# Kernel tuning notes

Measured on AMD Instinct MI355X. Metric: run time of the kernel, lower is better.

The kernel has to match this reference:

```python
import jax, jax.numpy as jnp
import numpy as np

B, S = 8, 1024          # 8 prefill sequences of length 1024, packed
HIDDEN = 4096
NH, NKV, HD = 32, 8, 128  # q heads, kv heads, head_dim = hidden // NH
G = NH // NKV             # GQA group size
NUM_BLOCKS, BLOCK_SIZE = 1024, 16
ROPE_THETA = 10000.0


def _apply_rope(q, k, pos):
    # q: [T, NH, HD], k: [T, NKV, HD], pos: [T] int32 (NeoX half-split rotation)
    half = HD // 2
    inv_freq = 1.0 / (ROPE_THETA ** (jnp.arange(0, HD, 2, dtype=jnp.float32) / HD))  # [half]
    ang = pos.astype(jnp.float32)[:, None] * inv_freq  # [T, half]
    cos = jnp.cos(ang)[:, None, :]  # [T, 1, half]
    sin = jnp.sin(ang)[:, None, :]

    def rot(t):
        t1, t2 = t[..., :half], t[..., half:]
        return jnp.concatenate([t1 * cos - t2 * sin, t2 * cos + t1 * sin], axis=-1)

    return rot(q), rot(k)


def setup_inputs() -> dict:
    key = jax.random.key(0)
    k1, k2, k3 = jax.random.split(key, 3)
    T = B * S
    x = jax.random.normal(k1, (T, HIDDEN), dtype=jnp.float32)
    wqkv = jax.random.normal(k2, (HIDDEN, (NH + 2 * NKV) * HD), dtype=jnp.float32) * 0.02
    bqkv = jnp.zeros(((NH + 2 * NKV) * HD,), dtype=jnp.float32)
    wo = jax.random.normal(k3, (NH * HD, HIDDEN), dtype=jnp.float32) * 0.02
    pos_list = jnp.tile(jnp.arange(S, dtype=jnp.int32), B)  # per-token position in its sequence
    # contiguous block allocation: token i of the packed batch -> cache slot i
    slot_mapping = jnp.arange(T, dtype=jnp.int32)  # block = slot // BLOCK_SIZE, offset = slot % BLOCK_SIZE
    k_cache = jnp.zeros((NUM_BLOCKS, BLOCK_SIZE, NKV, HD), dtype=jnp.float32)
    v_cache = jnp.zeros((NUM_BLOCKS, BLOCK_SIZE, NKV, HD), dtype=jnp.float32)
    return {"x": x, "wqkv": wqkv, "bqkv": bqkv, "wo": wo,
            "pos_list": pos_list, "slot_mapping": slot_mapping,
            "k_cache": k_cache, "v_cache": v_cache}


def reference(x, wqkv, bqkv, wo, pos_list, slot_mapping, k_cache, v_cache):
    scale = HD ** -0.5
    T = x.shape[0]
    qkv = x @ wqkv + bqkv  # [T, (NH+2*NKV)*HD]
    q = qkv[:, : NH * HD].reshape(T, NH, HD)
    k = qkv[:, NH * HD: (NH + NKV) * HD].reshape(T, NKV, HD)
    v = qkv[:, (NH + NKV) * HD:].reshape(T, NKV, HD)
    q, k = _apply_rope(q, k, pos_list)

    # varlen causal flash attention over B equal-length sequences (GQA)
    qb = q.reshape(B, S, NKV, G, HD)
    kb = k.reshape(B, S, NKV, HD)
    vb = v.reshape(B, S, NKV, HD)
    scores = jnp.einsum('bqhgd,bkhd->bhgqk', qb, kb) * scale  # [B,NKV,G,S,S]
    causal = jnp.tril(jnp.ones((S, S), dtype=bool))
    scores = jnp.where(causal, scores, jnp.float32(-1e30))
    probs = jax.nn.softmax(scores, axis=-1)
    out = jnp.einsum('bhgqk,bkhd->bqhgd', probs, vb).reshape(T, NH * HD)
    out = out @ wo  # [T, HIDDEN]

    # vectorized _write_to_paged_cache: scatter each token's k/v into its slot
    kc = k_cache.reshape(-1, NKV, HD).at[slot_mapping].set(k).reshape(k_cache.shape)
    vc = v_cache.reshape(-1, NKV, HD).at[slot_mapping].set(v).reshape(v_cache.shape)
    return out, kc, vc
```

## Files before the change

### kernel.cpp

```cpp
#include <hip/hip_runtime.h>

typedef unsigned short u16;
typedef unsigned int   u32;
typedef __attribute__((ext_vector_type(8))) short short8;
typedef __attribute__((ext_vector_type(4))) float f32x4;
typedef __attribute__((ext_vector_type(4))) u16   u16x4;

#define GLOAD16(gp, lp) __builtin_amdgcn_global_load_lds( \
    (const __attribute__((address_space(1))) void*)(gp),   \
    (__attribute__((address_space(3))) void*)(lp), 16, 0, 0)

__device__ __forceinline__ float bf2f(u16 u) {
  union { u32 i; float f; } v; v.i = ((u32)u) << 16; return v.f;
}
__device__ __forceinline__ u16 f2bf(float f) {
  union { float f; u32 i; } v; v.f = f;
  return (u16)((v.i + 0x7fffu + ((v.i >> 16) & 1u)) >> 16);
}

#define TTOK 8192
#define SLEN 1024
#define NBATCH 8
#define NHQ 32
#define NKVH 8
#define HDIM 128
#define QKVW 6144
#define HID 4096

__global__ void ap_copyf4(const f32x4* __restrict__ src, f32x4* __restrict__ dst, int n4) {
  int stride = gridDim.x * 256;
  for (int i = blockIdx.x * 256 + threadIdx.x; i < n4; i += stride) dst[i] = src[i];
}

__global__ void ap_convx(const float* __restrict__ x, u16* __restrict__ xb) {
  size_t e = ((size_t)blockIdx.x * 256 + threadIdx.x) * 8;
  f32x4 a = *(const f32x4*)(x + e);
  f32x4 b = *(const f32x4*)(x + e + 4);
  short8 o;
  o[0]=(short)f2bf(a[0]); o[1]=(short)f2bf(a[1]); o[2]=(short)f2bf(a[2]); o[3]=(short)f2bf(a[3]);
  o[4]=(short)f2bf(b[0]); o[5]=(short)f2bf(b[1]); o[6]=(short)f2bf(b[2]); o[7]=(short)f2bf(b[3]);
  *(short8*)(xb + e) = o;
}

__global__ __launch_bounds__(256) void ap_tconv(const float* __restrict__ src,
                                                u16* __restrict__ dst, int K, int N) {
  __shared__ u16 tile[64][68];
  int nt = N >> 6;
  int tn = blockIdx.x % nt, tk = blockIdx.x / nt;
  int rr = threadIdx.x >> 4, cc = (threadIdx.x & 15) * 4;
#pragma unroll
  for (int i = 0; i < 4; ++i) {
    int row = i * 16 + rr;
    f32x4 v = *(const f32x4*)(src + (size_t)(tk * 64 + row) * N + tn * 64 + cc);
#pragma unroll
    for (int j = 0; j < 4; ++j) tile[row][cc + j] = f2bf(v[j]);
  }
  __syncthreads();
#pragma unroll
  for (int i = 0; i < 4; ++i) {
    int orow = i * 16 + rr;
    u16x4 o;
#pragma unroll
    for (int j = 0; j < 4; ++j) o[j] = tile[cc + j][orow];
    *(u16x4*)(dst + (size_t)(tn * 64 + orow) * K + tk * 64 + cc) = o;
  }
}

__device__ __forceinline__ void ap_stage1k(const u16* __restrict__ g, int ldk,
                                           u16* __restrict__ l, int tid) {
#pragma unroll
  for (int i = 0; i < 2; ++i) {
    int ci = i * 1024 + tid;
    int r = ci >> 3;
    int cb = (ci & 7) * 16;
    int c = (cb ^ ((r & 7) << 4)) >> 1;
    GLOAD16(g + (size_t)r * ldk + c, l + ci * 8);
  }
}

__device__ __forceinline__ short8 ds_frag(const u16* base, int row, int kbyte, int swz) {
  return *(const short8*)((const char*)base + row * 128 + (kbyte ^ swz));
}

template <int OUT_BF16, int HAS_BIAS>
__global__ __launch_bounds__(1024) void ap_gemmw(const u16* __restrict__ A,
                                                 const u16* __restrict__ BT,
                                                 const float* __restrict__ bias,
                                                 void* __restrict__ Cout,
                                                 int M, int N, int K, int nbn) {
  __shared__ u16 sA[2][16384];
  __shared__ u16 sB[2][16384];
  const int tid = threadIdx.x;
  const int wave = tid >> 6, l = tid & 63, l16 = l & 15, lq = l >> 4;
  const int wr = wave >> 2, wc = wave & 3;
  const int swz = (l16 & 7) << 4;

  const int nwg = nbn * (M >> 8);
  const int cpx = nwg >> 3;
  const int wg = (blockIdx.x & 7) * cpx + (blockIdx.x >> 3);
  const int bm = wg / nbn, bn = wg % nbn;

  f32x4 acc[4][4];
  f32x4 zv = {0.f, 0.f, 0.f, 0.f};
#pragma unroll
  for (int mf = 0; mf < 4; ++mf)
#pragma unroll
    for (int nf = 0; nf < 4; ++nf) acc[mf][nf] = zv;

  const u16* Abase = A + (size_t)(bm * 256) * K;
  const u16* Bbase = BT + (size_t)(bn * 256) * K;
  const int NT = K >> 6;

  ap_stage1k(Abase, K, sA[0], tid);
  ap_stage1k(Bbase, K, sB[0], tid);

  for (int kt = 0; kt < NT; ++kt) {
    const u16* sAc = sA[kt & 1];
    const u16* sBc = sB[kt & 1];
    const bool pf = (kt + 1 < NT);

    if (pf) {
      ap_stage1k(Abase + (kt + 1) * 64, K, sA[(kt + 1) & 1], tid);
      ap_stage1k(Bbase + (kt + 1) * 64, K, sB[(kt + 1) & 1], tid);
      asm volatile("s_waitcnt vmcnt(4)" ::: "memory");
    } else {
      asm volatile("s_waitcnt vmcnt(0)" ::: "memory");
    }
    __builtin_amdgcn_s_barrier();
    __builtin_amdgcn_sched_barrier(0);

    {
      short8 bf_[4], af_[4];
#pragma unroll
      for (int nf = 0; nf < 4; ++nf)
        bf_[nf] = ds_frag(sBc, wc * 64 + nf * 16 + l16, lq * 16, swz);
#pragma unroll
      for (int mf = 0; mf < 4; ++mf)
        af_[mf] = ds_frag(sAc, wr * 64 + mf * 16 + l16, lq * 16, swz);
      asm volatile("s_waitcnt lgkmcnt(0)" ::: "memory");
      __builtin_amdgcn_sched_barrier(0);
      __builtin_amdgcn_s_setprio(1);
#pragma unroll
      for (int mf = 0; mf < 4; ++mf)
#pragma unroll
        for (int nf = 0; nf < 4; ++nf)
          acc[mf][nf] = __builtin_amdgcn_mfma_f32_16x16x32_bf16(
              af_[mf], bf_[nf], acc[mf][nf], 0, 0, 0);
      __builtin_amdgcn_s_setprio(0);
    }
    {
      short8 bf_[4], af_[4];
#pragma unroll
      for (int nf = 0; nf < 4; ++nf)
        bf_[nf] = ds_frag(sBc, wc * 64 + nf * 16 + l16, 64 + lq * 16, swz);
#pragma unroll
      for (int mf = 0; mf < 4; ++mf)
        af_[mf] = ds_frag(sAc, wr * 64 + mf * 16 + l16, 64 + lq * 16, swz);
      asm volatile("s_waitcnt lgkmcnt(0)" ::: "memory");
      __builtin_amdgcn_sched_barrier(0);
      __builtin_amdgcn_s_barrier();
      __builtin_amdgcn_s_setprio(1);
#pragma unroll
      for (int mf = 0; mf < 4; ++mf)
#pragma unroll
        for (int nf = 0; nf < 4; ++nf)
          acc[mf][nf] = __builtin_amdgcn_mfma_f32_16x16x32_bf16(
              af_[mf], bf_[nf], acc[mf][nf], 0, 0, 0);
      __builtin_amdgcn_s_setprio(0);
    }
  }

#pragma unroll
  for (int mf = 0; mf < 4; ++mf)
#pragma unroll
    for (int nf = 0; nf < 4; ++nf) {
      int col = bn * 256 + wc * 64 + nf * 16 + l16;
      float bv = HAS_BIAS ? bias[col] : 0.f;
#pragma unroll
      for (int r = 0; r < 4; ++r) {
        int row = bm * 256 + wr * 64 + mf * 16 + lq * 4 + r;
        float v = acc[mf][nf][r] + bv;
        if (OUT_BF16)
          ((u16*)Cout)[(size_t)row * N + col] = f2bf(v);
        else
          ((float*)Cout)[(size_t)row * N + col] = v;
      }
    }
}

__global__ __launch_bounds__(256) void ap_rope(u16* __restrict__ qkv,
                                               const int* __restrict__ pos_list,
                                               const int* __restrict__ slot_mapping,
                                               float* __restrict__ kc) {
  int gid = blockIdx.x * 4 + (threadIdx.x >> 6);
  int i = threadIdx.x & 63;
  int t = gid / 40, head = gid % 40;
  float pos = (float)pos_list[t];
  float inv = expf(-(float)i * 0.14391156516151135f);
  float ang = pos * inv;
  float cs = cosf(ang), sn = sinf(ang);
  int cb = (head < 32) ? head * 128 : 4096 + (head - 32) * 128;
  u16* p = qkv + (size_t)t * QKVW + cb;
  float t1 = bf2f(p[i]), t2 = bf2f(p[i + 64]);
  float o1 = t1 * cs - t2 * sn;
  float o2 = t2 * cs + t1 * sn;
  p[i] = f2bf(o1);
  p[i + 64] = f2bf(o2);
  if (head >= 32) {
    int slot = slot_mapping[t];
    float* kp = kc + (size_t)slot * (NKVH * HDIM) + (head - 32) * 128;
    kp[i] = o1;
    kp[i + 64] = o2;
  }
}

__global__ void ap_vscatter(const u16* __restrict__ qkv,
                            const int* __restrict__ slot_mapping,
                            float* __restrict__ vc) {
  int idx = blockIdx.x * 256 + threadIdx.x;
  int e = idx * 4;
  int t = e >> 10, r = e & 1023;
  int slot = slot_mapping[t];
  u16x4 v = *(const u16x4*)(qkv + (size_t)t * QKVW + 5120 + r);
  f32x4 o;
#pragma unroll
  for (int j = 0; j < 4; ++j) o[j] = bf2f(v[j]);
  *(f32x4*)(vc + (size_t)slot * 1024 + r) = o;
}

__global__ __launch_bounds__(256) void ap_vtrans(const u16* __restrict__ qkv,
                                                 u16* __restrict__ Vt) {
  __shared__ u16 tile[64][68];
  int bid = blockIdx.x;
  int hdt = bid & 1, st = (bid >> 1) & 15, head = bid >> 5;
  int b = head >> 3, h = head & 7;
  int rr = threadIdx.x >> 4, cc = (threadIdx.x & 15) * 4;
#pragma unroll
  for (int i = 0; i < 4; ++i) {
    int s = i * 16 + rr;
    u16x4 v = *(const u16x4*)(qkv + (size_t)(b * 1024 + st * 64 + s) * QKVW + 5120 +
                              h * 128 + hdt * 64 + cc);
#pragma unroll
    for (int j = 0; j < 4; ++j) tile[s][cc + j] = v[j];
  }
  __syncthreads();
#pragma unroll
  for (int i = 0; i < 4; ++i) {
    int hd = i * 16 + rr;
    u16x4 o;
#pragma unroll
    for (int j = 0; j < 4; ++j) o[j] = tile[cc + j][hd];
    *(u16x4*)(Vt + (size_t)head * (HDIM * SLEN) + (size_t)(hdt * 64 + hd) * SLEN +
              st * 64 + cc) = o;
  }
}

__global__ __launch_bounds__(512) void ap_attn4(const u16* __restrict__ qkv,
                                                const u16* __restrict__ Vt,
                                                u16* __restrict__ O) {
  __shared__ u16 sK[64 * 136];
  __shared__ u16 sV[128 * 72];
  __shared__ u16 sP[8 * 32 * 72];
  const int tid = threadIdx.x;
  const int wave = tid >> 6, l = tid & 63, l16 = l & 15, lq = l >> 4;
  const int bid = blockIdx.x;
  const int qt = bid & 15;
  const int kvh = (bid >> 4) & 7;
  const int b = bid >> 7;
  const int qh = kvh * 4 + (wave & 3);
  const int q0 = qt * 64 + (wave >> 2) * 32;
  const int head = b * 8 + kvh;
  const float SC2 = 0.12751649736230717f;

  short8 qf[2][4];
#pragma unroll
  for (int m = 0; m < 2; ++m)
#pragma unroll
    for (int kd = 0; kd < 4; ++kd) {
      size_t t = (size_t)(b * 1024 + q0 + m * 16 + l16);
      qf[m][kd] = *(const short8*)(qkv + t * QKVW + qh * 128 + kd * 32 + lq * 8);
    }

  u16* sPw = sP + wave * 2304;
  f32x4 zv = {0.f, 0.f, 0.f, 0.f};
  f32x4 oacc[2][8];
#pragma unroll
  for (int m = 0; m < 2; ++m)
#pragma unroll
    for (int n = 0; n < 8; ++n) oacc[m][n] = zv;
  float mrun[2][4], lrun[2][4];
#pragma unroll
  for (int m = 0; m < 2; ++m)
#pragma unroll
    for (int r = 0; r < 4; ++r) { mrun[m][r] = -1e30f; lrun[m][r] = 0.f; }

  const int ntiles = qt + 1;
  for (int kt = 0; kt < ntiles; ++kt) {
    const int kv0 = kt * 64;
#pragma unroll
    for (int i = 0; i < 2; ++i) {
      int ci = i * 512 + tid;
      int kr = ci >> 4, ko = (ci & 15) * 8;
      short8 v = *(const short8*)(qkv + (size_t)(b * 1024 + kv0 + kr) * QKVW + 4096 +
                                  kvh * 128 + ko);
      *(short8*)&sK[kr * 136 + ko] = v;
    }
#pragma unroll
    for (int i = 0; i < 2; ++i) {
      int ci = i * 512 + tid;
      int hd = ci >> 3, ko = (ci & 7) * 8;
      short8 v = *(const short8*)(Vt + (size_t)head * (HDIM * SLEN) + (size_t)hd * SLEN +
                                  kv0 + ko);
      *(short8*)&sV[hd * 72 + ko] = v;
    }
    __syncthreads();

    f32x4 sacc[2][4];
#pragma unroll
    for (int m = 0; m < 2; ++m)
#pragma unroll
      for (int nf = 0; nf < 4; ++nf) sacc[m][nf] = zv;
#pragma unroll
    for (int kd = 0; kd < 4; ++kd) {
      short8 kf[4];
#pragma unroll
      for (int nf = 0; nf < 4; ++nf)
        kf[nf] = *(const short8*)&sK[(nf * 16 + l16) * 136 + kd * 32 + lq * 8];
#pragma unroll
      for (int m = 0; m < 2; ++m)
#pragma unroll
        for (int nf = 0; nf < 4; ++nf)
          sacc[m][nf] = __builtin_amdgcn_mfma_f32_16x16x32_bf16(qf[m][kd], kf[nf], sacc[m][nf], 0, 0, 0);
    }
    if (kv0 + 63 > q0) {
#pragma unroll
      for (int m = 0; m < 2; ++m)
#pragma unroll
        for (int nf = 0; nf < 4; ++nf) {
          int kv = kv0 + nf * 16 + l16;
#pragma unroll
          for (int r = 0; r < 4; ++r) {
            int q = q0 + m * 16 + lq * 4 + r;
            if (kv > q) sacc[m][nf][r] = -1e30f;
          }
        }
    }
#pragma unroll
    for (int m = 0; m < 2; ++m)
#pragma unroll
      for (int r = 0; r < 4; ++r) {
        float mx = fmaxf(fmaxf(sacc[m][0][r], sacc[m][1][r]),
                         fmaxf(sacc[m][2][r], sacc[m][3][r]));
#pragma unroll
        for (int off = 8; off; off >>= 1) mx = fmaxf(mx, __shfl_xor(mx, off));
        float mn = fmaxf(mrun[m][r], mx);
        float sc = exp2f((mrun[m][r] - mn) * SC2);
        mrun[m][r] = mn;
        float p0 = exp2f((sacc[m][0][r] - mn) * SC2);
        float p1 = exp2f((sacc[m][1][r] - mn) * SC2);
        float p2 = exp2f((sacc[m][2][r] - mn) * SC2);
        float p3 = exp2f((sacc[m][3][r] - mn) * SC2);
        float rs = (p0 + p1) + (p2 + p3);
#pragma unroll
        for (int off = 8; off; off >>= 1) rs += __shfl_xor(rs, off);
        lrun[m][r] = lrun[m][r] * sc + rs;
#pragma unroll
        for (int n = 0; n < 8; ++n) oacc[m][n][r] *= sc;
        int prow = (m * 16 + lq * 4 + r) * 72;
        sPw[prow + l16]      = f2bf(p0);
        sPw[prow + 16 + l16] = f2bf(p1);
        sPw[prow + 32 + l16] = f2bf(p2);
        sPw[prow + 48 + l16] = f2bf(p3);
      }
    short8 pa[2][2];
#pragma unroll
    for (int m = 0; m < 2; ++m)
#pragma unroll
      for (int ks = 0; ks < 2; ++ks)
        pa[m][ks] = *(const short8*)&sPw[(m * 16 + l16) * 72 + ks * 32 + lq * 8];
#pragma unroll
    for (int n = 0; n < 8; ++n) {
#pragma unroll
      for (int ks = 0; ks < 2; ++ks) {
        short8 vb = *(const short8*)&sV[(n * 16 + l16) * 72 + ks * 32 + lq * 8];
#pragma unroll
        for (int m = 0; m < 2; ++m)
          oacc[m][n] = __builtin_amdgcn_mfma_f32_16x16x32_bf16(pa[m][ks], vb, oacc[m][n], 0, 0, 0);
      }
    }
    __syncthreads();
  }
#pragma unroll
  for (int m = 0; m < 2; ++m)
#pragma unroll
    for (int r = 0; r < 4; ++r) {
      float inv = 1.f / lrun[m][r];
      size_t t = (size_t)(b * 1024 + q0 + m * 16 + lq * 4 + r);
#pragma unroll
      for (int n = 0; n < 8; ++n)
        O[t * (size_t)HID + qh * 128 + n * 16 + l16] = f2bf(oacc[m][n][r] * inv);
    }
}

extern "C" void kernel_launch(void* const* d_in, const int* in_sizes, int n_in,
                              void* d_out, int out_size, void* d_ws, size_t ws_size,
                              hipStream_t stream) {
  const float* x = (const float*)d_in[0];
  const float* wqkv = (const float*)d_in[1];
  const float* bqkv = (const float*)d_in[2];
  const float* wo = (const float*)d_in[3];
  const int* pos_list = (const int*)d_in[4];
  const int* slot_mapping = (const int*)d_in[5];
  const float* k_cache = (const float*)d_in[6];
  const float* v_cache = (const float*)d_in[7];

  float* out = (float*)d_out;
  float* kc = out + (size_t)33554432;
  float* vc = kc + (size_t)16777216;

  char* ws = (char*)d_ws;
  u16* xb    = (u16*)(ws);
  u16* wqkvT = (u16*)(ws + 67108864);
  u16* woT   = (u16*)(ws + 117440512);
  u16* qkvb  = (u16*)(ws + 150994944);
  u16* Vt    = (u16*)(ws + 251658240);
  u16* attnO = xb;

  ap_copyf4<<<4096, 256, 0, stream>>>((const f32x4*)k_cache, (f32x4*)kc, 4194304);
  ap_copyf4<<<4096, 256, 0, stream>>>((const f32x4*)v_cache, (f32x4*)vc, 4194304);
  ap_convx<<<16384, 256, 0, stream>>>(x, xb);
  ap_tconv<<<6144, 256, 0, stream>>>(wqkv, wqkvT, 4096, 6144);
  ap_tconv<<<4096, 256, 0, stream>>>(wo, woT, 4096, 4096);
  ap_gemmw<1, 1><<<768, 1024, 0, stream>>>(xb, wqkvT, bqkv, qkvb, 8192, 6144, 4096, 24);
  ap_rope<<<81920, 256, 0, stream>>>(qkvb, pos_list, slot_mapping, kc);
  ap_vscatter<<<8192, 256, 0, stream>>>(qkvb, slot_mapping, vc);
  ap_vtrans<<<2048, 256, 0, stream>>>(qkvb, Vt);
  ap_attn4<<<1024, 512, 0, stream>>>(qkvb, Vt, attnO);
  ap_gemmw<0, 0><<<512, 1024, 0, stream>>>(attnO, woT, nullptr, out, 8192, 4096, 4096, 16);
}
```

Before: 1.139 ms.

## Prefetch both LDS fragment halves in GEMM and lazily rescale softmax in attention

In the GEMM main loop, the LDS fragment loads for both 64-wide K halves are now issued up front, and the first MFMA block waits only on the first half (lgkmcnt(8)). This overlaps LDS read latency of the second half with the first half's MFMAs. In attention, the online-softmax rescaling of the output accumulator and running sum now happens only when the row max grows by more than a threshold (FA4-style lazy rescale), skipping per-tile multiplies. The lazy rescale lets exponentials exceed 1 (up to 2^8), which changes rounding of the bf16 P values and holds more live registers.

```diff
diff --git a/kernel.cpp b/kernel.cpp
--- a/kernel.cpp
+++ b/kernel.cpp
@@ -129,45 +129,43 @@
     __builtin_amdgcn_s_barrier();
     __builtin_amdgcn_sched_barrier(0);
 
-    {
-      short8 bf_[4], af_[4];
+    short8 bf0[4], af0[4], bf1[4], af1[4];
+#pragma unroll
+    for (int nf = 0; nf < 4; ++nf)
+      bf0[nf] = ds_frag(sBc, wc * 64 + nf * 16 + l16, lq * 16, swz);
+#pragma unroll
+    for (int mf = 0; mf < 4; ++mf)
+      af0[mf] = ds_frag(sAc, wr * 64 + mf * 16 + l16, lq * 16, swz);
+    __builtin_amdgcn_sched_barrier(0);
+#pragma unroll
+    for (int nf = 0; nf < 4; ++nf)
+      bf1[nf] = ds_frag(sBc, wc * 64 + nf * 16 + l16, 64 + lq * 16, swz);
+#pragma unroll
+    for (int mf = 0; mf < 4; ++mf)
+      af1[mf] = ds_frag(sAc, wr * 64 + mf * 16 + l16, 64 + lq * 16, swz);
+
+    asm volatile("s_waitcnt lgkmcnt(8)" ::: "memory");
+    __builtin_amdgcn_sched_barrier(0);
+    __builtin_amdgcn_s_setprio(1);
+#pragma unroll
+    for (int mf = 0; mf < 4; ++mf)
 #pragma unroll
       for (int nf = 0; nf < 4; ++nf)
-        bf_[nf] = ds_frag(sBc, wc * 64 + nf * 16 + l16, lq * 16, swz);
-#pragma unroll
-      for (int mf = 0; mf < 4; ++mf)
-        af_[mf] = ds_frag(sAc, wr * 64 + mf * 16 + l16, lq * 16, swz);
-      asm volatile("s_waitcnt lgkmcnt(0)" ::: "memory");
-      __builtin_amdgcn_sched_barrier(0);
-      __builtin_amdgcn_s_setprio(1);
-#pragma unroll
-      for (int mf = 0; mf < 4; ++mf)
-#pragma unroll
-        for (int nf = 0; nf < 4; ++nf)
-          acc[mf][nf] = __builtin_amdgcn_mfma_f32_16x16x32_bf16(
-              af_[mf], bf_[nf], acc[mf][nf], 0, 0, 0);
-      __builtin_amdgcn_s_setprio(0);
-    }
-    {
-      short8 bf_[4], af_[4];
+        acc[mf][nf] = __builtin_amdgcn_mfma_f32_16x16x32_bf16(
+            af0[mf], bf0[nf], acc[mf][nf], 0, 0, 0);
+    __builtin_amdgcn_s_setprio(0);
+
+    asm volatile("s_waitcnt lgkmcnt(0)" ::: "memory");
+    __builtin_amdgcn_sched_barrier(0);
+    __builtin_amdgcn_s_barrier();
+    __builtin_amdgcn_s_setprio(1);
+#pragma unroll
+    for (int mf = 0; mf < 4; ++mf)
 #pragma unroll
       for (int nf = 0; nf < 4; ++nf)
-        bf_[nf] = ds_frag(sBc, wc * 64 + nf * 16 + l16, 64 + lq * 16, swz);
-#pragma unroll
-      for (int mf = 0; mf < 4; ++mf)
-        af_[mf] = ds_frag(sAc, wr * 64 + mf * 16 + l16, 64 + lq * 16, swz);
-      asm volatile("s_waitcnt lgkmcnt(0)" ::: "memory");
-      __builtin_amdgcn_sched_barrier(0);
-      __builtin_amdgcn_s_barrier();
-      __builtin_amdgcn_s_setprio(1);
-#pragma unroll
-      for (int mf = 0; mf < 4; ++mf)
-#pragma unroll
-        for (int nf = 0; nf < 4; ++nf)
-          acc[mf][nf] = __builtin_amdgcn_mfma_f32_16x16x32_bf16(
-              af_[mf], bf_[nf], acc[mf][nf], 0, 0, 0);
-      __builtin_amdgcn_s_setprio(0);
-    }
+        acc[mf][nf] = __builtin_amdgcn_mfma_f32_16x16x32_bf16(
+            af1[mf], bf1[nf], acc[mf][nf], 0, 0, 0);
+    __builtin_amdgcn_s_setprio(0);
   }
 
 #pragma unroll
@@ -255,7 +253,7 @@
   }
 }
 
-__global__ __launch_bounds__(512) void ap_attn4(const u16* __restrict__ qkv,
+__global__ __launch_bounds__(512) void ap_attn5(const u16* __restrict__ qkv,
                                                 const u16* __restrict__ Vt,
                                                 u16* __restrict__ O) {
   __shared__ u16 sK[64 * 136];
@@ -353,9 +351,14 @@
                          fmaxf(sacc[m][2][r], sacc[m][3][r]));
 #pragma unroll
         for (int off = 8; off; off >>= 1) mx = fmaxf(mx, __shfl_xor(mx, off));
-        float mn = fmaxf(mrun[m][r], mx);
-        float sc = exp2f((mrun[m][r] - mn) * SC2);
-        mrun[m][r] = mn;
+        if ((mx - mrun[m][r]) * SC2 > 8.f) {
+          float sc = exp2f((mrun[m][r] - mx) * SC2);
+          mrun[m][r] = mx;
+          lrun[m][r] *= sc;
+#pragma unroll
+          for (int n = 0; n < 8; ++n) oacc[m][n][r] *= sc;
+        }
+        float mn = mrun[m][r];
         float p0 = exp2f((sacc[m][0][r] - mn) * SC2);
         float p1 = exp2f((sacc[m][1][r] - mn) * SC2);
         float p2 = exp2f((sacc[m][2][r] - mn) * SC2);
@@ -363,9 +366,7 @@
         float rs = (p0 + p1) + (p2 + p3);
 #pragma unroll
         for (int off = 8; off; off >>= 1) rs += __shfl_xor(rs, off);
-        lrun[m][r] = lrun[m][r] * sc + rs;
-#pragma unroll
-        for (int n = 0; n < 8; ++n) oacc[m][n][r] *= sc;
+        lrun[m][r] += rs;
         int prow = (m * 16 + lq * 4 + r) * 72;
         sPw[prow + l16]      = f2bf(p0);
         sPw[prow + 16 + l16] = f2bf(p1);
@@ -435,6 +436,6 @@
   ap_rope<<<81920, 256, 0, stream>>>(qkvb, pos_list, slot_mapping, kc);
   ap_vscatter<<<8192, 256, 0, stream>>>(qkvb, slot_mapping, vc);
   ap_vtrans<<<2048, 256, 0, stream>>>(qkvb, Vt);
-  ap_attn4<<<1024, 512, 0, stream>>>(qkvb, Vt, attnO);
+  ap_attn5<<<1024, 512, 0, stream>>>(qkvb, Vt, attnO);
   ap_gemmw<0, 0><<<512, 1024, 0, stream>>>(attnO, woT, nullptr, out, 8192, 4096, 4096, 16);
 }
```

New measurement: 1.958 ms. 71.9% more time.
